# Optimization experiments

Measured on AMD Instinct MI355X. Metric: run time of the kernel, lower is better.

Reference implementation:

```python
import jax, jax.numpy as jnp
import numpy as np

N_NODES = 50000
N_EDGES = 800000
IN_C = 64
OUT_C = 64
K = 4  # spectral coefficients; weight has K+1 slices (selfconn)
EPS = 1e-16  # PyG segment-softmax epsilon


def setup_inputs() -> dict:
    key = jax.random.key(0)
    k1, k2, k3, k4, k5 = jax.random.split(key, 5)
    x = jax.random.normal(k1, (N_NODES, IN_C), dtype=jnp.float32)
    edge_index = jax.random.randint(k2, (2, N_EDGES), 0, N_NODES, dtype=jnp.int64)
    edge_attr = jax.random.normal(k3, (N_EDGES, K), dtype=jnp.float32)
    # glorot-style scale for weight [K+1, in, out]
    stdv = np.sqrt(6.0 / (IN_C + OUT_C))
    weight = jax.random.uniform(k4, (K + 1, IN_C, OUT_C), dtype=jnp.float32,
                                minval=-stdv, maxval=stdv)
    bias = jnp.zeros((OUT_C,), dtype=jnp.float32)
    att_vector = jax.random.normal(k5, (IN_C, 1), dtype=jnp.float32) * 0.1
    return {"x": x, "edge_attr": edge_attr, "weight": weight, "bias": bias,
            "att_vector": att_vector, "edge_index": edge_index}


def _segment_softmax(logits, seg, num_segments):
    mx = jax.ops.segment_max(logits, seg, num_segments=num_segments)
    ex = jnp.exp(logits - mx[seg])
    den = jax.ops.segment_sum(ex, seg, num_segments=num_segments)
    return ex / (den[seg] + EPS)


def reference(x, edge_attr, weight, bias, att_vector, edge_index):
    src, dst = edge_index[0], edge_index[1]
    n_nodes = x.shape[0]
    # messages for all K coefficients at once: [E, K, C]
    msgs = edge_attr[:, :, None] * x[src][:, None, :]
    # sum branch: per-k scatter_add then per-k weight -> fused einsum
    sum_agg = jax.ops.segment_sum(msgs, dst, num_segments=n_nodes)  # [N, K, C]
    sum_out = x @ weight[-1] + jnp.einsum('nkc,kco->no', sum_agg, weight[:K])
    # attention branch
    pooled = msgs.mean(axis=1)                       # [E, C]
    raw_att = (pooled @ att_vector)[:, 0]            # [E]
    att_scores = _segment_softmax(raw_att, dst, n_nodes)
    att_agg = jax.ops.segment_sum(att_scores[:, None, None] * msgs, dst,
                                  num_segments=n_nodes)  # [N, K, C]
    out = sum_out + jnp.einsum('nkc,kco->no', att_agg, weight[:K]) + bias
    return out, att_scores
```

## Files before the change

kernel.cpp:

```cpp
#include <hip/hip_runtime.h>
#include <math.h>

#define C 64
#define KCOEF 4
#define FN 128
#define FK 64
#define APAD 65

#define BSH 7
#define RN 128
#define CAP 2560
#define EPB 16
#define MAXNBK 512

__global__ __launch_bounds__(256) void kAH(const float* __restrict__ x,
        const float* __restrict__ attv, const int* __restrict__ dst,
        float* __restrict__ dvec, int* __restrict__ deg, int N, int E, int NBD) {
    if ((int)blockIdx.x < NBD) {
        int t = threadIdx.x;
        int n = blockIdx.x * 16 + (t >> 4);
        int q = t & 15;
        if (n >= N) return;
        float4 xv = *(const float4*)(x + (size_t)n * C + q * 4);
        float4 av = *(const float4*)(attv + q * 4);
        float p = xv.x * av.x + xv.y * av.y + xv.z * av.z + xv.w * av.w;
        #pragma unroll
        for (int o = 8; o > 0; o >>= 1) p += __shfl_xor(p, o, 16);
        if (q == 0) dvec[n] = p;
    } else {
        int e = ((int)blockIdx.x - NBD) * 256 + (int)threadIdx.x;
        if (e >= E) return;
        atomicAdd(&deg[dst[e]], 1);
    }
}

__global__ __launch_bounds__(256) void kS1(const int* __restrict__ deg,
        int* __restrict__ off, int* __restrict__ bsum, int N) {
    int g = blockIdx.x * 256 + threadIdx.x;
    int lane = threadIdx.x & 63, w = threadIdx.x >> 6;
    int v = (g < N) ? deg[g] : 0;
    int incl = v;
    #pragma unroll
    for (int s = 1; s < 64; s <<= 1) {
        int t = __shfl_up(incl, s);
        if (lane >= s) incl += t;
    }
    __shared__ int wtot[4];
    if (lane == 63) wtot[w] = incl;
    __syncthreads();
    int add = 0;
    for (int ww = 0; ww < w; ++ww) add += wtot[ww];
    int excl = incl - v + add;
    if (g < N) off[g] = excl;
    if (threadIdx.x == 255) bsum[blockIdx.x] = excl + v;
}

__global__ __launch_bounds__(256) void kS2(int* __restrict__ bsum, int NB) {
    int t = threadIdx.x;
    int lane = t & 63, w = t >> 6;
    int v = (t < NB) ? bsum[t] : 0;
    int incl = v;
    #pragma unroll
    for (int s = 1; s < 64; s <<= 1) {
        int tt = __shfl_up(incl, s);
        if (lane >= s) incl += tt;
    }
    __shared__ int wtot[4];
    if (lane == 63) wtot[w] = incl;
    __syncthreads();
    int add = 0;
    for (int ww = 0; ww < w; ++ww) add += wtot[ww];
    if (t < NB) bsum[t] = incl - v + add;
}

__global__ __launch_bounds__(256) void kS3(int* __restrict__ off,
        const int* __restrict__ bsum, int* __restrict__ gcur, int N, int E) {
    int g = blockIdx.x * 256 + threadIdx.x;
    if (g == 0) off[N] = E;
    if (g >= N) return;
    int o = off[g] + bsum[blockIdx.x];
    off[g] = o;
    if ((g & (RN - 1)) == 0) gcur[g >> BSH] = o;
}

__global__ __launch_bounds__(256) void kBIN(const int* __restrict__ src,
        const int* __restrict__ dst, const float* __restrict__ ea,
        const float* __restrict__ dvec, int* __restrict__ gcur,
        float4* __restrict__ pay, int E, int NBK) {
    __shared__ int hist[MAXNBK];
    __shared__ int cursor[MAXNBK];
    int tid = threadIdx.x;
    int base = blockIdx.x * (256 * EPB);
    for (int b = tid; b < NBK; b += 256) hist[b] = 0;
    __syncthreads();
    int bb[EPB];
    #pragma unroll
    for (int i = 0; i < EPB; ++i) {
        int e = base + i * 256 + tid;
        bb[i] = -1;
        if (e < E) {
            bb[i] = dst[e] >> BSH;
            atomicAdd(&hist[bb[i]], 1);
        }
    }
    __syncthreads();
    for (int b = tid; b < NBK; b += 256) cursor[b] = atomicAdd(&gcur[b], hist[b]);
    __syncthreads();
    #pragma unroll
    for (int i = 0; i < EPB; ++i) {
        int e = base + i * 256 + tid;
        if (e < E) {
            int sN = src[e];
            int d  = dst[e];
            float4 a = ((const float4*)ea)[e];
            float mean = (a.x + a.y + a.z + a.w) * 0.25f;
            float r = mean * dvec[sN];
            int p = atomicAdd(&cursor[bb[i]], 1);
            float4 q0 = make_float4(r, __int_as_float(sN * (C * 4)), a.x, a.y);
            float4 q1 = make_float4(a.z, a.w, __int_as_float(d & (RN - 1)), 0.f);
            pay[(size_t)p * 2]     = q0;
            pay[(size_t)p * 2 + 1] = q1;
        }
    }
}

__global__ __launch_bounds__(512) void kAGG(const float* __restrict__ x,
        const float4* __restrict__ pay, const int* __restrict__ off,
        float* __restrict__ mA, float* __restrict__ invA,
        float* __restrict__ agg, int N) {
    __shared__ float  rA[CAP];
    __shared__ int    xoA[CAP];
    __shared__ float4 qA[CAP];
    __shared__ int    no[RN + 1];
    __shared__ int    ncur[RN];
    int tid = threadIdx.x;
    int nb = blockIdx.x;
    int n0 = nb << BSH;
    int n1 = min(n0 + RN, N);
    int nn = n1 - n0;
    int bstart = off[n0];
    int cnt = off[n1] - bstart;
    if (cnt > CAP) cnt = CAP;
    if (tid <= nn) {
        int o = off[n0 + tid] - bstart;
        no[tid] = o;
        if (tid < nn) ncur[tid] = o;
    }
    __syncthreads();
    for (int i = tid; i < cnt; i += 512) {
        float4 p0 = pay[(size_t)(bstart + i) * 2];
        float4 p1 = pay[(size_t)(bstart + i) * 2 + 1];
        int dl = __float_as_int(p1.z);
        int p = atomicAdd(&ncur[dl], 1);
        rA[p]  = p0.x;
        xoA[p] = __float_as_int(p0.y);
        qA[p]  = make_float4(p0.z, p0.w, p1.x, p1.y);
    }
    __syncthreads();
    int wv = tid >> 6, lane = tid & 63;
    const char* xb = (const char*)x + (size_t)lane * 4;
    for (int nl = wv; nl < nn; nl += 8) {
        int s = no[nl];
        int d = no[nl + 1] - s;
        int n = n0 + nl;
        size_t ab = (size_t)n * (KCOEF * C) + lane;
        if (d == 0) {
            agg[ab] = 0.f; agg[ab + 64] = 0.f; agg[ab + 128] = 0.f; agg[ab + 192] = 0.f;
            if (lane == 0) { mA[n] = 0.f; invA[n] = 1.f; }
            continue;
        }
        float m = -INFINITY;
        for (int i = lane; i < d; i += 64) m = fmaxf(m, rA[s + i]);
        #pragma unroll
        for (int o = 32; o > 0; o >>= 1) m = fmaxf(m, __shfl_xor(m, o));
        float ss = 0.f;
        for (int i = lane; i < d; i += 64) ss += expf(rA[s + i] - m);
        #pragma unroll
        for (int o = 32; o > 0; o >>= 1) ss += __shfl_xor(ss, o);
        float inv = 1.f / (ss + 1e-16f);
        if (lane == 0) { mA[n] = m; invA[n] = inv; }
        float a0 = 0.f, a1 = 0.f, a2 = 0.f, a3 = 0.f;
        #pragma unroll 2
        for (int j = 0; j < d; ++j) {
            float rj = rA[s + j];
            float4 q = qA[s + j];
            int ob = xoA[s + j];
            float w = 1.f + expf(rj - m) * inv;
            float xr = *(const float*)(xb + ob);
            float wx = w * xr;
            a0 = fmaf(q.x, wx, a0);
            a1 = fmaf(q.y, wx, a1);
            a2 = fmaf(q.z, wx, a2);
            a3 = fmaf(q.w, wx, a3);
        }
        agg[ab] = a0; agg[ab + 64] = a1; agg[ab + 128] = a2; agg[ab + 192] = a3;
    }
}

__global__ __launch_bounds__(256) void kF3(const float* __restrict__ agg,
        const float* __restrict__ x, const float* __restrict__ W,
        const float* __restrict__ bias, float* __restrict__ out_node, int N) {
    __shared__ float As[FN][APAD];
    __shared__ float Ws[FK][C];
    int tid = threadIdx.x;
    int nbase = blockIdx.x * FN;
    int ng = tid >> 3;
    int cg = tid & 7;
    float4 acc0[4], acc1[4];
    #pragma unroll
    for (int j = 0; j < 4; ++j) { acc0[j] = {0,0,0,0}; acc1[j] = {0,0,0,0}; }

    int srow_q = tid & 15;
    int srow_b = tid >> 4;

    for (int k0 = 0; k0 < 320; k0 += FK) {
        #pragma unroll
        for (int pass = 0; pass < 8; ++pass) {
            int row = pass * 16 + srow_b;
            int n = nbase + row; if (n >= N) n = N - 1;
            float4 v;
            if (k0 < 256) v = *(const float4*)(agg + (size_t)n * 256 + k0 + srow_q * 4);
            else          v = *(const float4*)(x   + (size_t)n * C   + srow_q * 4);
            As[row][srow_q * 4 + 0] = v.x;
            As[row][srow_q * 4 + 1] = v.y;
            As[row][srow_q * 4 + 2] = v.z;
            As[row][srow_q * 4 + 3] = v.w;
        }
        #pragma unroll
        for (int p = 0; p < 4; ++p) {
            int idx = tid + p * 256;
            ((float4*)Ws)[idx] = ((const float4*)(W + (size_t)k0 * C))[idx];
        }
        __syncthreads();
        #pragma unroll 2
        for (int i = 0; i < FK; ++i) {
            float a0 = As[ng * 4 + 0][i];
            float a1 = As[ng * 4 + 1][i];
            float a2 = As[ng * 4 + 2][i];
            float a3 = As[ng * 4 + 3][i];
            float4 w0 = *(const float4*)&Ws[i][cg * 8];
            float4 w1 = *(const float4*)&Ws[i][cg * 8 + 4];
            acc0[0].x = fmaf(a0, w0.x, acc0[0].x); acc0[0].y = fmaf(a0, w0.y, acc0[0].y);
            acc0[0].z = fmaf(a0, w0.z, acc0[0].z); acc0[0].w = fmaf(a0, w0.w, acc0[0].w);
            acc1[0].x = fmaf(a0, w1.x, acc1[0].x); acc1[0].y = fmaf(a0, w1.y, acc1[0].y);
            acc1[0].z = fmaf(a0, w1.z, acc1[0].z); acc1[0].w = fmaf(a0, w1.w, acc1[0].w);
            acc0[1].x = fmaf(a1, w0.x, acc0[1].x); acc0[1].y = fmaf(a1, w0.y, acc0[1].y);
            acc0[1].z = fmaf(a1, w0.z, acc0[1].z); acc0[1].w = fmaf(a1, w0.w, acc0[1].w);
            acc1[1].x = fmaf(a1, w1.x, acc1[1].x); acc1[1].y = fmaf(a1, w1.y, acc1[1].y);
            acc1[1].z = fmaf(a1, w1.z, acc1[1].z); acc1[1].w = fmaf(a1, w1.w, acc1[1].w);
            acc0[2].x = fmaf(a2, w0.x, acc0[2].x); acc0[2].y = fmaf(a2, w0.y, acc0[2].y);
            acc0[2].z = fmaf(a2, w0.z, acc0[2].z); acc0[2].w = fmaf(a2, w0.w, acc0[2].w);
            acc1[2].x = fmaf(a2, w1.x, acc1[2].x); acc1[2].y = fmaf(a2, w1.y, acc1[2].y);
            acc1[2].z = fmaf(a2, w1.z, acc1[2].z); acc1[2].w = fmaf(a2, w1.w, acc1[2].w);
            acc0[3].x = fmaf(a3, w0.x, acc0[3].x); acc0[3].y = fmaf(a3, w0.y, acc0[3].y);
            acc0[3].z = fmaf(a3, w0.z, acc0[3].z); acc0[3].w = fmaf(a3, w0.w, acc0[3].w);
            acc1[3].x = fmaf(a3, w1.x, acc1[3].x); acc1[3].y = fmaf(a3, w1.y, acc1[3].y);
            acc1[3].z = fmaf(a3, w1.z, acc1[3].z); acc1[3].w = fmaf(a3, w1.w, acc1[3].w);
        }
        __syncthreads();
    }
    float4 bA = *(const float4*)(bias + cg * 8);
    float4 bB = *(const float4*)(bias + cg * 8 + 4);
    #pragma unroll
    for (int j = 0; j < 4; ++j) {
        int n = nbase + ng * 4 + j;
        if (n < N) {
            float4 oA = { acc0[j].x + bA.x, acc0[j].y + bA.y, acc0[j].z + bA.z, acc0[j].w + bA.w };
            float4 oB = { acc1[j].x + bB.x, acc1[j].y + bB.y, acc1[j].z + bB.z, acc1[j].w + bB.w };
            *(float4*)(out_node + (size_t)n * C + cg * 8)     = oA;
            *(float4*)(out_node + (size_t)n * C + cg * 8 + 4) = oB;
        }
    }
}

__global__ __launch_bounds__(256) void kT(const int* __restrict__ src,
        const int* __restrict__ dst, const float* __restrict__ ea,
        const float* __restrict__ dvec, const float* __restrict__ mA,
        const float* __restrict__ invA, float* __restrict__ out_att, int E) {
    int e = blockIdx.x * 256 + threadIdx.x;
    if (e >= E) return;
    float4 a = ((const float4*)ea)[e];
    float mean = (a.x + a.y + a.z + a.w) * 0.25f;
    float r = mean * dvec[src[e]];
    int d = dst[e];
    out_att[e] = expf(r - mA[d]) * invA[d];
}

extern "C" void kernel_launch(void* const* d_in, const int* in_sizes, int n_in,
                              void* d_out, int out_size, void* d_ws, size_t ws_size,
                              hipStream_t stream) {
    const float* x    = (const float*)d_in[0];
    const float* ea   = (const float*)d_in[1];
    const float* W    = (const float*)d_in[2];
    const float* bias = (const float*)d_in[3];
    const float* attv = (const float*)d_in[4];
    const int*   ei   = (const int*)d_in[5];

    int N = in_sizes[0] / C;
    int E = in_sizes[5] / 2;
    const int* src = ei;
    const int* dst = ei + E;

    float* out_node = (float*)d_out;
    float* out_att  = (float*)d_out + (size_t)N * C;

    char* ws = (char*)d_ws;
    float* agg  = (float*)ws; ws += (size_t)N * KCOEF * C * sizeof(float);
    float4* pay = (float4*)ws; ws += (size_t)E * 32;
    float* dvec = (float*)ws; ws += (size_t)N * sizeof(float);
    int*   deg  = (int*)ws;   ws += (size_t)N * sizeof(int);
    int*   off  = (int*)ws;   ws += (size_t)(N + 1) * sizeof(int);
    float* mA   = (float*)ws; ws += (size_t)N * sizeof(float);
    int*   gcur = (int*)ws;   ws += MAXNBK * sizeof(int);
    int*   bsum = (int*)ws;   ws += 1024;

    float* invA = (float*)deg;

    int NB  = (N + 255) / 256;
    int NBD = (N + 15) / 16;
    int NBH = (E + 255) / 256;
    int NBK = (N + RN - 1) >> BSH;
    int NBB = (E + 256 * EPB - 1) / (256 * EPB);
    int NBF = (N + FN - 1) / FN;

    hipMemsetAsync(deg, 0, (size_t)N * sizeof(int), stream);
    kAH  <<<NBD + NBH, 256, 0, stream>>>(x, attv, dst, dvec, deg, N, E, NBD);
    kS1  <<<NB, 256, 0, stream>>>(deg, off, bsum, N);
    kS2  <<<1, 256, 0, stream>>>(bsum, NB);
    kS3  <<<NB, 256, 0, stream>>>(off, bsum, gcur, N, E);
    kBIN <<<NBB, 256, 0, stream>>>(src, dst, ea, dvec, gcur, pay, E, NBK);
    kAGG <<<NBK, 512, 0, stream>>>(x, pay, off, mA, invA, agg, N);
    kF3  <<<NBF, 256, 0, stream>>>(agg, x, W, bias, out_node, N);
    kT   <<<NBH, 256, 0, stream>>>(src, dst, ea, dvec, mA, invA, out_att, E);
}
```

Baseline: 278.3 us.

## Halve node bins and precompute softmax weights per edge in aggregation kernel

Bins shrink from 128 to 64 nodes, with 256-thread aggregation blocks. The local destination index is packed into the high bits of the source-offset word, so the payload slot no longer carries it. Aggregation now runs a separate softmax-statistics pass, then converts each edge's logit into its final weight once in shared memory. Before, all 64 lanes recomputed the same exp per edge inside the gather loop. The bit packing assumes byte offsets under 2^24 and bins of at most 64 nodes, and adds two extra block barriers.

```diff
diff --git a/kernel.cpp b/kernel.cpp
--- a/kernel.cpp
+++ b/kernel.cpp
@@ -7,11 +7,11 @@
 #define FK 64
 #define APAD 65
 
-#define BSH 7
-#define RN 128
-#define CAP 2560
-#define EPB 16
-#define MAXNBK 512
+#define BSH 6
+#define RN 64
+#define CAP 1280
+#define EPB 32
+#define MAXNBK 1024
 
 __global__ __launch_bounds__(256) void kAH(const float* __restrict__ x,
         const float* __restrict__ attv, const int* __restrict__ dst,
@@ -93,20 +93,13 @@
     int base = blockIdx.x * (256 * EPB);
     for (int b = tid; b < NBK; b += 256) hist[b] = 0;
     __syncthreads();
-    int bb[EPB];
-    #pragma unroll
     for (int i = 0; i < EPB; ++i) {
         int e = base + i * 256 + tid;
-        bb[i] = -1;
-        if (e < E) {
-            bb[i] = dst[e] >> BSH;
-            atomicAdd(&hist[bb[i]], 1);
-        }
+        if (e < E) atomicAdd(&hist[dst[e] >> BSH], 1);
     }
     __syncthreads();
     for (int b = tid; b < NBK; b += 256) cursor[b] = atomicAdd(&gcur[b], hist[b]);
     __syncthreads();
-    #pragma unroll
     for (int i = 0; i < EPB; ++i) {
         int e = base + i * 256 + tid;
         if (e < E) {
@@ -115,16 +108,17 @@
             float4 a = ((const float4*)ea)[e];
             float mean = (a.x + a.y + a.z + a.w) * 0.25f;
             float r = mean * dvec[sN];
-            int p = atomicAdd(&cursor[bb[i]], 1);
-            float4 q0 = make_float4(r, __int_as_float(sN * (C * 4)), a.x, a.y);
-            float4 q1 = make_float4(a.z, a.w, __int_as_float(d & (RN - 1)), 0.f);
+            int p = atomicAdd(&cursor[d >> BSH], 1);
+            int xo = ((d & (RN - 1)) << 24) | (sN << 8);
+            float4 q0 = make_float4(r, __int_as_float(xo), a.x, a.y);
+            float4 q1 = make_float4(a.z, a.w, 0.f, 0.f);
             pay[(size_t)p * 2]     = q0;
             pay[(size_t)p * 2 + 1] = q1;
         }
     }
 }
 
-__global__ __launch_bounds__(512) void kAGG(const float* __restrict__ x,
+__global__ __launch_bounds__(256) void kAGG(const float* __restrict__ x,
         const float4* __restrict__ pay, const int* __restrict__ off,
         float* __restrict__ mA, float* __restrict__ invA,
         float* __restrict__ agg, int N) {
@@ -133,9 +127,9 @@
     __shared__ float4 qA[CAP];
     __shared__ int    no[RN + 1];
     __shared__ int    ncur[RN];
+    __shared__ float  mL[RN], ivL[RN];
     int tid = threadIdx.x;
-    int nb = blockIdx.x;
-    int n0 = nb << BSH;
+    int n0 = (int)blockIdx.x << BSH;
     int n1 = min(n0 + RN, N);
     int nn = n1 - n0;
     int bstart = off[n0];
@@ -143,49 +137,59 @@
     if (cnt > CAP) cnt = CAP;
     if (tid <= nn) {
         int o = off[n0 + tid] - bstart;
+        o = min(o, CAP);
         no[tid] = o;
         if (tid < nn) ncur[tid] = o;
     }
     __syncthreads();
-    for (int i = tid; i < cnt; i += 512) {
+    for (int i = tid; i < cnt; i += 256) {
         float4 p0 = pay[(size_t)(bstart + i) * 2];
         float4 p1 = pay[(size_t)(bstart + i) * 2 + 1];
-        int dl = __float_as_int(p1.z);
-        int p = atomicAdd(&ncur[dl], 1);
+        int v = __float_as_int(p0.y);
+        int p = atomicAdd(&ncur[v >> 24], 1);
         rA[p]  = p0.x;
-        xoA[p] = __float_as_int(p0.y);
+        xoA[p] = v;
         qA[p]  = make_float4(p0.z, p0.w, p1.x, p1.y);
     }
     __syncthreads();
     int wv = tid >> 6, lane = tid & 63;
+    for (int nl = wv; nl < nn; nl += 4) {
+        int s = no[nl];
+        int d = no[nl + 1] - s;
+        int n = n0 + nl;
+        if (d == 0) {
+            if (lane == 0) { mL[nl] = 0.f; ivL[nl] = 1.f; mA[n] = 0.f; invA[n] = 1.f; }
+            continue;
+        }
+        float m = -INFINITY;
+        for (int i = lane; i < d; i += 64) m = fmaxf(m, rA[s + i]);
+        #pragma unroll
+        for (int o = 32; o > 0; o >>= 1) m = fmaxf(m, __shfl_xor(m, o));
+        float ss = 0.f;
+        for (int i = lane; i < d; i += 64) ss += expf(rA[s + i] - m);
+        #pragma unroll
+        for (int o = 32; o > 0; o >>= 1) ss += __shfl_xor(ss, o);
+        float inv = 1.f / (ss + 1e-16f);
+        if (lane == 0) { mL[nl] = m; ivL[nl] = inv; mA[n] = m; invA[n] = inv; }
+    }
+    __syncthreads();
+    for (int i = tid; i < cnt; i += 256) {
+        int dl = xoA[i] >> 24;
+        rA[i] = 1.f + expf(rA[i] - mL[dl]) * ivL[dl];
+    }
+    __syncthreads();
     const char* xb = (const char*)x + (size_t)lane * 4;
-    for (int nl = wv; nl < nn; nl += 8) {
+    for (int nl = wv; nl < nn; nl += 4) {
         int s = no[nl];
         int d = no[nl + 1] - s;
         int n = n0 + nl;
         size_t ab = (size_t)n * (KCOEF * C) + lane;
-        if (d == 0) {
-            agg[ab] = 0.f; agg[ab + 64] = 0.f; agg[ab + 128] = 0.f; agg[ab + 192] = 0.f;
-            if (lane == 0) { mA[n] = 0.f; invA[n] = 1.f; }
-            continue;
-        }
-        float m = -INFINITY;
-        for (int i = lane; i < d; i += 64) m = fmaxf(m, rA[s + i]);
-        #pragma unroll
-        for (int o = 32; o > 0; o >>= 1) m = fmaxf(m, __shfl_xor(m, o));
-        float ss = 0.f;
-        for (int i = lane; i < d; i += 64) ss += expf(rA[s + i] - m);
-        #pragma unroll
-        for (int o = 32; o > 0; o >>= 1) ss += __shfl_xor(ss, o);
-        float inv = 1.f / (ss + 1e-16f);
-        if (lane == 0) { mA[n] = m; invA[n] = inv; }
         float a0 = 0.f, a1 = 0.f, a2 = 0.f, a3 = 0.f;
-        #pragma unroll 2
+        #pragma unroll 4
         for (int j = 0; j < d; ++j) {
-            float rj = rA[s + j];
+            float w = rA[s + j];
             float4 q = qA[s + j];
-            int ob = xoA[s + j];
-            float w = 1.f + expf(rj - m) * inv;
+            int ob = xoA[s + j] & 0xFFFFFF;
             float xr = *(const float*)(xb + ob);
             float wx = w * xr;
             a0 = fmaf(q.x, wx, a0);
@@ -329,7 +333,7 @@
     kS2  <<<1, 256, 0, stream>>>(bsum, NB);
     kS3  <<<NB, 256, 0, stream>>>(off, bsum, gcur, N, E);
     kBIN <<<NBB, 256, 0, stream>>>(src, dst, ea, dvec, gcur, pay, E, NBK);
-    kAGG <<<NBK, 512, 0, stream>>>(x, pay, off, mA, invA, agg, N);
+    kAGG <<<NBK, 256, 0, stream>>>(x, pay, off, mA, invA, agg, N);
     kF3  <<<NBF, 256, 0, stream>>>(agg, x, W, bias, out_node, N);
     kT   <<<NBH, 256, 0, stream>>>(src, dst, ea, dvec, mA, invA, out_att, E);
 }
```

Result: slower. 290.4 us (+4.4%).
